# Optimization experiments

Hardware: AMD Instinct MI355X
Metric: run time of the kernel (lower is better)

## Reference

```python
import jax, jax.numpy as jnp
import numpy as np

B, C, CQK, H, W = 4, 256, 64, 64, 64


def setup_inputs() -> dict:
    key = jax.random.key(0)
    ks = jax.random.split(key, 8)
    scale = 1.0 / np.sqrt(C)
    features = jax.random.normal(ks[0], (B, C, H, W), dtype=jnp.float32)
    Wq = jax.random.normal(ks[1], (CQK, C), dtype=jnp.float32) * scale
    bq = jax.random.normal(ks[2], (CQK,), dtype=jnp.float32) * 0.01
    Wk = jax.random.normal(ks[3], (CQK, C), dtype=jnp.float32) * scale
    bk = jax.random.normal(ks[4], (CQK,), dtype=jnp.float32) * 0.01
    Wv = jax.random.normal(ks[5], (C, C), dtype=jnp.float32) * scale
    bv = jax.random.normal(ks[6], (C,), dtype=jnp.float32) * 0.01
    # nn.Parameter(torch.zeros(1)) in the original; use a nonzero value so the
    # attention path contributes to the output (and gradients) during testing.
    weight = jax.random.normal(ks[7], (1,), dtype=jnp.float32) * 0.5
    return {"features": features, "Wq": Wq, "bq": bq, "Wk": Wk, "bk": bk,
            "Wv": Wv, "bv": bv, "weight": weight}


def reference(features, Wq, bq, Wk, bk, Wv, bv, weight):
    b, c, h, w = features.shape
    x = features.reshape(b, c, h * w)                       # [B, C, N]
    # 1x1 convs == channel-mixing matmuls
    q = jnp.einsum('oc,bcn->bon', Wq, x) + bq[None, :, None]  # [B, CQK, N]
    k = jnp.einsum('oc,bcn->bon', Wk, x) + bk[None, :, None]  # [B, CQK, N]
    v = jnp.einsum('oc,bcn->bon', Wv, x) + bv[None, :, None]  # [B, C, N]
    # energy[b,i,j] = <q[:, i], k[:, j]>; softmax over keys j
    energy = jnp.einsum('bci,bcj->bij', q, k)                 # [B, N, N]
    attention = jax.nn.softmax(energy, axis=-1)
    # out[b,c,i] = sum_j v[b,c,j] * attention[b,i,j]
    out = jnp.einsum('bcj,bij->bci', v, attention)            # [B, C, N]
    return (weight[0] * out + x).reshape(b, c, h, w)
```

## Files before the change

kernel.cpp:

```cpp
#include <hip/hip_runtime.h>
#include <hip/hip_bf16.h>

constexpr int BB  = 4;
constexpr int CC  = 256;
constexpr int CQ  = 64;
constexpr int NN  = 4096;
constexpr int KS  = 4;
constexpr int QTR = 128;
constexpr int KVB = 32;

typedef __attribute__((ext_vector_type(8))) short bf16x8;
typedef __attribute__((ext_vector_type(4))) float f32x4;

__device__ __forceinline__ short f2bf(float f) {
    unsigned u = __float_as_uint(f);
    unsigned r = u + 0x7fffu + ((u >> 16) & 1u);
    return (short)(r >> 16);
}

__device__ __forceinline__ short f2bf_fast(float f) {
    __bf16 h = (__bf16)f;
    return *reinterpret_cast<short*>(&h);
}

__device__ __forceinline__ void gload16(const void* gsrc, void* ldst) {
    __builtin_amdgcn_global_load_lds(
        (const __attribute__((address_space(1))) unsigned int*)gsrc,
        (__attribute__((address_space(3))) unsigned int*)ldst, 16, 0, 0);
}

__global__ __launch_bounds__(256, 3) void proj_kernel(
        const float* __restrict__ x,
        const float* __restrict__ Wq, const float* __restrict__ bq,
        const float* __restrict__ Wk, const float* __restrict__ bk,
        const float* __restrict__ Wv, const float* __restrict__ bv,
        short* __restrict__ Qt, short* __restrict__ Kt,
        short* __restrict__ Vm) {
    const int id  = blockIdx.x;
    const int xcd = id & 7, sub = id >> 3;
    const int b   = xcd >> 1;
    const int og  = sub >> 4;
    const int ntl = ((xcd & 1) << 4) + (sub & 15);
    const int n0  = ntl * 128;

    const int t    = threadIdx.x;
    const int wv   = t >> 6;
    const int lane = t & 63;
    const int l15  = lane & 15;
    const int g    = lane >> 4;

    __shared__ __align__(16) short Wl[64 * 256];
    __shared__ __align__(16) short Xl[2][128 * 40];

    const float* Wsrc; const float* bsrc; float scale;
    if (og == 0)      { Wsrc = Wq;                  bsrc = bq;               scale = 1.4426950408889634f; }
    else if (og == 1) { Wsrc = Wk;                  bsrc = bk;               scale = 1.0f; }
    else              { Wsrc = Wv + (og - 2) * 64 * 256; bsrc = bv + (og - 2) * 64; scale = 1.0f; }

    {
        const int oc = t >> 2, kb = (t & 3) * 64;
        const float* wr = Wsrc + oc * 256 + kb;
#pragma unroll
        for (int cc = 0; cc < 8; ++cc) {
            bf16x8 wchunk;
#pragma unroll
            for (int e = 0; e < 8; ++e) wchunk[e] = f2bf_fast(wr[cc * 8 + e] * scale);
            const int c = (kb >> 3) + cc;
            char* dst = (char*)Wl + oc * 512 + ((c * 16) ^ ((oc & 7) << 4));
            *(bf16x8*)dst = wchunk;
        }
    }

    const int xn   = t & 127;
    const int half = t >> 7;
    const float* xb = x + (size_t)b * CC * NN + n0 + xn;
    const int swn  = ((xn & 3) ^ ((xn >> 3) & 3));

    auto stageX = [&](int kc, int buf) {
        const float* xr = xb + (size_t)(kc * 32 + half * 16) * NN;
        float v[16];
#pragma unroll
        for (int kk = 0; kk < 16; ++kk) v[kk] = xr[(size_t)kk * NN];
#pragma unroll
        for (int cc = 0; cc < 2; ++cc) {
            bf16x8 pk;
#pragma unroll
            for (int e = 0; e < 8; ++e) pk[e] = f2bf_fast(v[cc * 8 + e]);
            const int c = half * 2 + cc;
            char* dst = (char*)&Xl[buf][0] + xn * 80 + ((c ^ swn) << 4);
            *(bf16x8*)dst = pk;
        }
    };

    f32x4 acc[8];
#pragma unroll
    for (int nf = 0; nf < 8; ++nf) acc[nf] = (f32x4){0.f, 0.f, 0.f, 0.f};

    stageX(0, 0);

    const int ocr = wv * 16 + l15;
    for (int kc = 0; kc < 8; ++kc) {
        __syncthreads();
        if (kc < 7) stageX(kc + 1, (kc + 1) & 1);

        const char* wsrcl = (const char*)Wl + ocr * 512
                          + (((kc * 4 + g) * 16) ^ ((ocr & 7) << 4));
        bf16x8 af = *(const bf16x8*)wsrcl;

        const char* xbase = (const char*)&Xl[kc & 1][0];
#pragma unroll
        for (int nf = 0; nf < 8; ++nf) {
            const int n = nf * 16 + l15;
            const int swr = ((n & 3) ^ ((n >> 3) & 3));
            bf16x8 bf = *(const bf16x8*)(xbase + n * 80 + ((g ^ swr) << 4));
            acc[nf] = __builtin_amdgcn_mfma_f32_16x16x32_bf16(af, bf, acc[nf], 0, 0, 0);
        }
    }

    float bias4[4];
#pragma unroll
    for (int r = 0; r < 4; ++r) bias4[r] = bsrc[wv * 16 + g * 4 + r] * scale;

    if (og < 2) {
        short* base = (og == 0 ? Qt : Kt) + (size_t)b * NN * 64;
#pragma unroll
        for (int nf = 0; nf < 8; ++nf) {
            const int n = n0 + nf * 16 + l15;
            short4 pk;
            pk.x = f2bf_fast(acc[nf][0] + bias4[0]);
            pk.y = f2bf_fast(acc[nf][1] + bias4[1]);
            pk.z = f2bf_fast(acc[nf][2] + bias4[2]);
            pk.w = f2bf_fast(acc[nf][3] + bias4[3]);
            *(short4*)(base + (size_t)n * 64 + wv * 16 + g * 4) = pk;
        }
    } else {
        short* vb = Vm + (size_t)b * CC * NN;
        const int c0 = (og - 2) * 64 + wv * 16 + g * 4;
#pragma unroll
        for (int nf = 0; nf < 8; ++nf) {
            const int n = n0 + nf * 16 + l15;
#pragma unroll
            for (int r = 0; r < 4; ++r)
                vb[(size_t)(c0 + r) * NN + n] = f2bf_fast(acc[nf][r] + bias4[r]);
        }
    }
}

__global__ __launch_bounds__(256, 2) void flash_kernel(
        const short* __restrict__ Qt, const short* __restrict__ Kt,
        const short* __restrict__ Vm,
        short* __restrict__ Opart, float* __restrict__ Lp) {
    const int id  = blockIdx.x;
    const int xcd = id & 7, sub = id >> 3;
    const int b   = xcd >> 1;
    const int qt  = sub & 31;
    const int ks  = ((xcd & 1) << 1) | (sub >> 5);

    const int wave = threadIdx.x >> 6;
    const int lane = threadIdx.x & 63;
    const int l15  = lane & 15;
    const int g    = lane >> 4;

    __shared__ short Kl[2][KVB * 64];
    __shared__ short Vl[2][CC * KVB];

    const short* Qb = Qt + (size_t)b * NN * 64;
    const short* Kb = Kt + (size_t)b * NN * 64;
    const short* Vb = Vm + (size_t)b * CC * NN;

    const int qbase = qt * QTR + wave * 32;

    bf16x8 qf[2][2];
#pragma unroll
    for (int rf = 0; rf < 2; ++rf)
#pragma unroll
        for (int kk = 0; kk < 2; ++kk)
            qf[rf][kk] = *(const bf16x8*)(Qb + (size_t)(qbase + rf * 16 + l15) * 64
                                          + kk * 32 + g * 8);

    float lsum_p[2] = {0.0f, 0.0f};

    f32x4 oacc[2][16];
#pragma unroll
    for (int rf = 0; rf < 2; ++rf)
#pragma unroll
        for (int ch = 0; ch < 16; ++ch) oacc[rf][ch] = (f32x4){0.f, 0.f, 0.f, 0.f};

    const int vrow_off = lane >> 2;
    const int vscol    = (((lane & 3) ^ ((lane >> 3) & 3)) << 4);
    const int krow_off = lane >> 3;
    const int kscol    = (((lane & 7) ^ (lane >> 3)) << 4);

    auto stage = [&](int buf, int kbase) {
#pragma unroll
        for (int i = 0; i < 5; ++i) {
            const int s = wave * 5 + i;
            if (s < 16) {
                const int row = s * 16 + vrow_off;
                const char* src = (const char*)(Vb + (size_t)row * NN + kbase) + vscol;
                gload16(src, (char*)&Vl[buf][0] + s * 1024);
            } else {
                const int ss = s - 16;
                const int j  = ss * 8 + krow_off;
                const int sj = (((j & 15) >> 2) << 3) + ((j >> 4) << 2) + (j & 3);
                const char* src = (const char*)(Kb + (size_t)(kbase + sj) * 64) + kscol;
                gload16(src, (char*)&Kl[buf][0] + ss * 1024);
            }
        }
    };

    const int kt0 = ks * (NN / KS);
    stage(0, kt0);

    for (int it = 0; it < NN / KS / KVB; ++it) {
        const int cur = it & 1;
        __syncthreads();
        if (it < NN / KS / KVB - 1) stage(cur ^ 1, kt0 + (it + 1) * KVB);

        f32x4 s2[2][2];
#pragma unroll
        for (int jt = 0; jt < 2; ++jt) {
            const int krow = jt * 16 + l15;
            const int sw   = (krow & 7) << 4;
            const char* kr = (const char*)&Kl[cur][0] + krow * 128;
            bf16x8 kf0 = *(const bf16x8*)(kr + ((g * 16) ^ sw));
            bf16x8 kf1 = *(const bf16x8*)(kr + ((64 + g * 16) ^ sw));
#pragma unroll
            for (int rf = 0; rf < 2; ++rf) {
                f32x4 a = (f32x4){0.f, 0.f, 0.f, 0.f};
                a = __builtin_amdgcn_mfma_f32_16x16x32_bf16(kf0, qf[rf][0], a, 0, 0, 0);
                a = __builtin_amdgcn_mfma_f32_16x16x32_bf16(kf1, qf[rf][1], a, 0, 0, 0);
                s2[rf][jt] = a;
            }
        }

        bf16x8 pf[2];
#pragma unroll
        for (int rf = 0; rf < 2; ++rf) {
#pragma unroll
            for (int jt = 0; jt < 2; ++jt)
#pragma unroll
                for (int r = 0; r < 4; ++r) {
                    float p = exp2f(s2[rf][jt][r]);
                    lsum_p[rf] += p;
                    pf[rf][jt * 4 + r] = f2bf_fast(p);
                }
        }

        __builtin_amdgcn_s_setprio(1);
#pragma unroll
        for (int ch = 0; ch < 16; ++ch) {
            const int vrow = ch * 16 + l15;
            const int col  = (g * 16) ^ (((vrow >> 1) & 3) << 4);
            bf16x8 vf = *(const bf16x8*)((const char*)&Vl[cur][0] + vrow * 64 + col);
#pragma unroll
            for (int rf = 0; rf < 2; ++rf)
                oacc[rf][ch] = __builtin_amdgcn_mfma_f32_16x16x32_bf16(pf[rf], vf,
                                                                       oacc[rf][ch], 0, 0, 0);
        }
        __builtin_amdgcn_s_setprio(0);
    }

    const int pt = (b * 32 + qt) * KS + ks;
    short* Op = Opart + (size_t)pt * QTR * 256;
#pragma unroll
    for (int rf = 0; rf < 2; ++rf)
#pragma unroll
        for (int ch = 0; ch < 16; ++ch)
#pragma unroll
            for (int r = 0; r < 4; ++r)
                Op[(size_t)(wave * 32 + rf * 16 + g * 4 + r) * 256 + ch * 16 + l15] =
                    f2bf_fast(oacc[rf][ch][r]);
#pragma unroll
    for (int rf = 0; rf < 2; ++rf) {
        float v = lsum_p[rf];
        v += __shfl_xor(v, 16);
        v += __shfl_xor(v, 32);
        if (lane < 16)
            Lp[(size_t)pt * QTR + wave * 32 + rf * 16 + lane] = v;
    }
}

__global__ __launch_bounds__(256) void combine_kernel(
        const short* __restrict__ Opart, const float* __restrict__ Lp,
        const float* __restrict__ x, const float* __restrict__ weightp,
        float* __restrict__ out) {
    const int b     = blockIdx.x;
    const int rowg0 = blockIdx.y * 32;
    const int qt    = rowg0 >> 7;
    const int rbase = rowg0 & 127;
    const int t     = threadIdx.x;

    __shared__ float oc[32][257];
    __shared__ float linv[32];

    const int pt0 = (b * 32 + qt) * KS;

    if (t < 32) {
        const size_t mb = (size_t)pt0 * QTR + rbase + t;
        float L = 0.f;
#pragma unroll
        for (int s = 0; s < KS; ++s) L += Lp[mb + (size_t)s * QTR];
        linv[t] = 1.0f / L;
    }
    __syncthreads();

    const size_t ob = (size_t)pt0 * QTR * 256 + (size_t)rbase * 256;
#pragma unroll 4
    for (int row = 0; row < 32; ++row) {
        float acc = 0.f;
#pragma unroll
        for (int s = 0; s < KS; ++s) {
            unsigned u = (unsigned)(unsigned short)
                Opart[ob + (size_t)s * QTR * 256 + row * 256 + t];
            acc += __uint_as_float(u << 16);
        }
        oc[row][t] = acc * linv[row];
    }
    __syncthreads();

    const float wgt = weightp[0];
    const int row = t & 31, cg = t >> 5;
    const float* xb = x + (size_t)b * CC * NN + rowg0 + row;
    float* op = out + (size_t)b * CC * NN + rowg0 + row;
#pragma unroll 4
    for (int c = cg; c < 256; c += 8) {
        op[(size_t)c * NN] = wgt * oc[row][c] + xb[(size_t)c * NN];
    }
}

extern "C" void kernel_launch(void* const* d_in, const int* in_sizes, int n_in,
                              void* d_out, int out_size, void* d_ws, size_t ws_size,
                              hipStream_t stream) {
    const float* feat = (const float*)d_in[0];
    const float* Wq   = (const float*)d_in[1];
    const float* bq   = (const float*)d_in[2];
    const float* Wk   = (const float*)d_in[3];
    const float* bk   = (const float*)d_in[4];
    const float* Wv   = (const float*)d_in[5];
    const float* bv   = (const float*)d_in[6];
    const float* wgt  = (const float*)d_in[7];
    float* out = (float*)d_out;

    short* Qt = (short*)d_ws;
    short* Kt = Qt + (size_t)BB * NN * CQ;
    short* Vm = Kt + (size_t)BB * NN * CQ;
    short* Opart = Vm + (size_t)BB * CC * NN;
    float* Lp = (float*)(Opart + (size_t)BB * 32 * KS * QTR * 256);

    proj_kernel<<<dim3(768), 256, 0, stream>>>(
        feat, Wq, bq, Wk, bk, Wv, bv, Qt, Kt, Vm);

    flash_kernel<<<dim3(BB * 32 * KS), 256, 0, stream>>>(
        Qt, Kt, Vm, Opart, Lp);

    combine_kernel<<<dim3(BB, NN / 32), 256, 0, stream>>>(
        Opart, Lp, feat, wgt, out);
}
```

Baseline: 85.53 us.

## Split flash waves into 2x2 row/channel grid with 16x16x16 PV MFMA

Reorganizes the four waves of each flash block from 32 query rows by all 256 channels into a 2x2 grid: each wave now owns 64 query rows and 128 channels. The QK scores are computed in 16-key halves, and P is fed straight into the 16x16x16 bf16 MFMA for PV, so the K row permutation in staging goes away. Each wave now reads only half of the V tile from LDS while reusing it across twice as many query rows, which cuts LDS traffic per MFMA. In exchange the QK^T and exp work is duplicated across the two channel-group waves, and PV uses the smaller K=16 MFMA instead of K=32.

```diff
diff --git a/kernel.cpp b/kernel.cpp
--- a/kernel.cpp
+++ b/kernel.cpp
@@ -10,6 +10,7 @@
 constexpr int KVB = 32;
 
 typedef __attribute__((ext_vector_type(8))) short bf16x8;
+typedef __attribute__((ext_vector_type(4))) short bf16x4;
 typedef __attribute__((ext_vector_type(4))) float f32x4;
 
 __device__ __forceinline__ short f2bf(float f) {
@@ -157,6 +158,8 @@
     const int ks  = ((xcd & 1) << 1) | (sub >> 5);
 
     const int wave = threadIdx.x >> 6;
+    const int rg   = wave >> 1;
+    const int cg   = wave & 1;
     const int lane = threadIdx.x & 63;
     const int l15  = lane & 15;
     const int g    = lane >> 4;
@@ -168,23 +171,29 @@
     const short* Kb = Kt + (size_t)b * NN * 64;
     const short* Vb = Vm + (size_t)b * CC * NN;
 
-    const int qbase = qt * QTR + wave * 32;
-
-    bf16x8 qf[2][2];
-#pragma unroll
-    for (int rf = 0; rf < 2; ++rf)
+    const int qbase = qt * QTR + rg * 64;
+
+    bf16x8 qf[4][2];
+#pragma unroll
+    for (int rf = 0; rf < 4; ++rf)
 #pragma unroll
         for (int kk = 0; kk < 2; ++kk)
             qf[rf][kk] = *(const bf16x8*)(Qb + (size_t)(qbase + rf * 16 + l15) * 64
                                           + kk * 32 + g * 8);
 
-    float lsum_p[2] = {0.0f, 0.0f};
-
-    f32x4 oacc[2][16];
-#pragma unroll
-    for (int rf = 0; rf < 2; ++rf)
-#pragma unroll
-        for (int ch = 0; ch < 16; ++ch) oacc[rf][ch] = (f32x4){0.f, 0.f, 0.f, 0.f};
+    float lsum_p[4] = {0.f, 0.f, 0.f, 0.f};
+
+    f32x4 oacc[4][8];
+#pragma unroll
+    for (int rf = 0; rf < 4; ++rf)
+#pragma unroll
+        for (int chf = 0; chf < 8; ++chf) oacc[rf][chf] = (f32x4){0.f, 0.f, 0.f, 0.f};
+
+    const int k_off0 = l15 * 128 + ((g * 16)      ^ ((l15 & 7) << 4));
+    const int k_off1 = l15 * 128 + ((64 + g * 16) ^ ((l15 & 7) << 4));
+    const int vswz   = ((l15 >> 1) & 3) << 4;
+    const int v_offA = l15 * 64 + (((g >> 1) << 4) ^ vswz) + (g & 1) * 8;
+    const int v_offB = l15 * 64 + ((((g >> 1) + 2) << 4) ^ vswz) + (g & 1) * 8;
 
     const int vrow_off = lane >> 2;
     const int vscol    = (((lane & 3) ^ ((lane >> 3) & 3)) << 4);
@@ -201,9 +210,8 @@
                 gload16(src, (char*)&Vl[buf][0] + s * 1024);
             } else {
                 const int ss = s - 16;
-                const int j  = ss * 8 + krow_off;
-                const int sj = (((j & 15) >> 2) << 3) + ((j >> 4) << 2) + (j & 3);
-                const char* src = (const char*)(Kb + (size_t)(kbase + sj) * 64) + kscol;
+                const int key = kbase + ss * 8 + krow_off;
+                const char* src = (const char*)(Kb + (size_t)key * 64) + kscol;
                 gload16(src, (char*)&Kl[buf][0] + ss * 1024);
             }
         }
@@ -217,67 +225,60 @@
         __syncthreads();
         if (it < NN / KS / KVB - 1) stage(cur ^ 1, kt0 + (it + 1) * KVB);
 
-        f32x4 s2[2][2];
-#pragma unroll
-        for (int jt = 0; jt < 2; ++jt) {
-            const int krow = jt * 16 + l15;
-            const int sw   = (krow & 7) << 4;
-            const char* kr = (const char*)&Kl[cur][0] + krow * 128;
-            bf16x8 kf0 = *(const bf16x8*)(kr + ((g * 16) ^ sw));
-            bf16x8 kf1 = *(const bf16x8*)(kr + ((64 + g * 16) ^ sw));
-#pragma unroll
-            for (int rf = 0; rf < 2; ++rf) {
+        const char* klb = (const char*)&Kl[cur][0];
+        const char* vlb = (const char*)&Vl[cur][0] + cg * 8192;
+
+#pragma unroll
+        for (int h = 0; h < 2; ++h) {
+            const char* kr = klb + h * 2048;
+            bf16x8 kf0 = *(const bf16x8*)(kr + k_off0);
+            bf16x8 kf1 = *(const bf16x8*)(kr + k_off1);
+            bf16x4 pf[4];
+#pragma unroll
+            for (int rf = 0; rf < 4; ++rf) {
                 f32x4 a = (f32x4){0.f, 0.f, 0.f, 0.f};
                 a = __builtin_amdgcn_mfma_f32_16x16x32_bf16(kf0, qf[rf][0], a, 0, 0, 0);
                 a = __builtin_amdgcn_mfma_f32_16x16x32_bf16(kf1, qf[rf][1], a, 0, 0, 0);
-                s2[rf][jt] = a;
+#pragma unroll
+                for (int r = 0; r < 4; ++r) {
+                    float p = exp2f(a[r]);
+                    lsum_p[rf] += p;
+                    pf[rf][r] = f2bf_fast(p);
+                }
             }
-        }
-
-        bf16x8 pf[2];
-#pragma unroll
-        for (int rf = 0; rf < 2; ++rf) {
-#pragma unroll
-            for (int jt = 0; jt < 2; ++jt)
-#pragma unroll
-                for (int r = 0; r < 4; ++r) {
-                    float p = exp2f(s2[rf][jt][r]);
-                    lsum_p[rf] += p;
-                    pf[rf][jt * 4 + r] = f2bf_fast(p);
-                }
-        }
-
-        __builtin_amdgcn_s_setprio(1);
-#pragma unroll
-        for (int ch = 0; ch < 16; ++ch) {
-            const int vrow = ch * 16 + l15;
-            const int col  = (g * 16) ^ (((vrow >> 1) & 3) << 4);
-            bf16x8 vf = *(const bf16x8*)((const char*)&Vl[cur][0] + vrow * 64 + col);
-#pragma unroll
-            for (int rf = 0; rf < 2; ++rf)
-                oacc[rf][ch] = __builtin_amdgcn_mfma_f32_16x16x32_bf16(pf[rf], vf,
-                                                                       oacc[rf][ch], 0, 0, 0);
-        }
-        __builtin_amdgcn_s_setprio(0);
+            const int v_off = h ? v_offB : v_offA;
+            __builtin_amdgcn_s_setprio(1);
+#pragma unroll
+            for (int chf = 0; chf < 8; ++chf) {
+                bf16x4 vf = *(const bf16x4*)(vlb + chf * 1024 + v_off);
+#pragma unroll
+                for (int rf = 0; rf < 4; ++rf)
+                    oacc[rf][chf] = __builtin_amdgcn_mfma_f32_16x16x16bf16_1k(
+                        pf[rf], vf, oacc[rf][chf], 0, 0, 0);
+            }
+            __builtin_amdgcn_s_setprio(0);
+        }
     }
 
     const int pt = (b * 32 + qt) * KS + ks;
     short* Op = Opart + (size_t)pt * QTR * 256;
 #pragma unroll
-    for (int rf = 0; rf < 2; ++rf)
-#pragma unroll
-        for (int ch = 0; ch < 16; ++ch)
+    for (int rf = 0; rf < 4; ++rf)
+#pragma unroll
+        for (int chf = 0; chf < 8; ++chf)
 #pragma unroll
             for (int r = 0; r < 4; ++r)
-                Op[(size_t)(wave * 32 + rf * 16 + g * 4 + r) * 256 + ch * 16 + l15] =
-                    f2bf_fast(oacc[rf][ch][r]);
-#pragma unroll
-    for (int rf = 0; rf < 2; ++rf) {
-        float v = lsum_p[rf];
-        v += __shfl_xor(v, 16);
-        v += __shfl_xor(v, 32);
-        if (lane < 16)
-            Lp[(size_t)pt * QTR + wave * 32 + rf * 16 + lane] = v;
+                Op[(size_t)(rg * 64 + rf * 16 + g * 4 + r) * 256
+                   + cg * 128 + chf * 16 + l15] = f2bf_fast(oacc[rf][chf][r]);
+    if (cg == 0) {
+#pragma unroll
+        for (int rf = 0; rf < 4; ++rf) {
+            float v = lsum_p[rf];
+            v += __shfl_xor(v, 16);
+            v += __shfl_xor(v, 32);
+            if (lane < 16)
+                Lp[(size_t)pt * QTR + rg * 64 + rf * 16 + lane] = v;
+        }
     }
 }
 
```

New measurement: 118.1 us. +38.1%, slower.
